# Kernel tuning notes

Measured on AMD Instinct MI355X. Metric: run time of the kernel, lower is better.

The kernel has to match this reference:

```python
import jax, jax.numpy as jnp
import numpy as np

SYM_LIST = np.array([12, 15, 18, 19, 20], dtype=np.int32)   # symmetric class ids (dataset.get_sym_list())
SELECT_ID = np.arange(1, 31, dtype=np.int32)                 # self.select_id = [1..30]
STEP = 20                                                     # pixel subsampling stride
SCORING_WEIGHT = 0.01


def quat_to_mat(q):
    """Exact translation of get_loss.quaternion_matrix. q: [..., 4] -> [..., 3, 3]."""
    q0, q1, q2, q3 = q[..., 0], q[..., 1], q[..., 2], q[..., 3]
    R = jnp.stack([
        1.0 - 2.0 * (q2 ** 2 + q3 ** 2), 2.0 * q1 * q2 - 2.0 * q0 * q3, 2.0 * q0 * q2 + 2.0 * q1 * q3,
        2.0 * q1 * q2 + 2.0 * q3 * q0, 1.0 - 2.0 * (q1 ** 2 + q3 ** 2), -2.0 * q0 * q1 + 2.0 * q2 * q3,
        -2.0 * q0 * q2 + 2.0 * q1 * q3, 2.0 * q0 * q1 + 2.0 * q2 * q3, 1.0 - 2.0 * (q1 ** 2 + q2 ** 2),
    ], axis=-1)
    return R.reshape(q.shape[:-1] + (3, 3))


def setup_inputs() -> dict:
    key = jax.random.key(0)
    ks = jax.random.split(key, 7)
    bs, h, w, P = 8, 64, 64, 400
    pred_r = jax.random.normal(ks[0], (bs, 4, h, w), jnp.float32)
    pred_t = jax.random.normal(ks[1], (bs, 3, h, w), jnp.float32) * 0.1
    pred_score = jax.random.uniform(ks[2], (bs, h, w), jnp.float32, 1e-3, 1.0)
    gt_r = jax.random.normal(ks[3], (bs, 3, 3), jnp.float32)
    gt_t = jax.random.normal(ks[4], (bs, 3), jnp.float32) * 0.1
    cls_ids = jax.random.randint(ks[5], (bs,), 0, 30, jnp.int32)
    model_xyz = jax.random.normal(ks[6], (bs, 3, P), jnp.float32) * 0.05
    return {"pred_r": pred_r, "pred_t": pred_t, "pred_score": pred_score,
            "gt_r": gt_r, "gt_t": gt_t, "cls_ids": cls_ids, "model_xyz": model_xyz}


def reference(pred_r, pred_t, pred_score, gt_r, gt_t, cls_ids, model_xyz):
    bs, _, h, w = pred_r.shape
    hw = h * w
    # per-pixel quaternion normalization
    pred_r = pred_r / jnp.linalg.norm(pred_r, axis=1, keepdims=True)
    pr = pred_r.reshape(bs, 4, hw)
    pt = pred_t.reshape(bs, 3, hw)
    ps = pred_score.reshape(bs, hw)
    # static strided subsampling of valid pixels (full mask -> every STEP-th pixel)
    V = hw // STEP
    idx = jnp.arange(V) * STEP
    pr = pr[:, :, idx]                 # [bs,4,V]
    pt = pt[:, :, idx]                 # [bs,3,V]
    ps = ps[:, idx]                    # [bs,V]
    R_pre = quat_to_mat(jnp.moveaxis(pr, 1, 2))                       # [bs,V,3,3]
    # transformed model points per valid pixel
    pred = jnp.einsum('bvij,bjp->bvip', R_pre, model_xyz) \
        + jnp.moveaxis(pt, 1, 2)[..., None]                           # [bs,V,3,P]
    gt = jnp.einsum('bij,bjp->bip', gt_r, model_xyz) + gt_t[..., None]  # [bs,3,P]
    # ADD: same-index point distances
    add = jnp.mean(jnp.linalg.norm(pred - gt[:, None], axis=2), axis=2)  # [bs,V]
    # ADD-S: nearest-neighbor (knn_one_point + gather == min over gt points)
    pn = jnp.sum(pred ** 2, axis=2)                                    # [bs,V,P]
    gn = jnp.sum(gt ** 2, axis=1)                                      # [bs,P]
    cross = jnp.einsum('bvip,biq->bvpq', pred, gt)                     # [bs,V,P,P]
    d2 = pn[..., None] + gn[:, None, None, :] - 2.0 * cross
    adds = jnp.mean(jnp.sqrt(jnp.maximum(jnp.min(d2, axis=-1), 0.0)), axis=2)  # [bs,V]
    is_sym = jnp.isin(cls_ids, jnp.asarray(SYM_LIST))                  # [bs]
    add_ij = jnp.where(is_sym[:, None], adds, add)                     # [bs,V]
    valid = jnp.isin(cls_ids + 1, jnp.asarray(SELECT_ID))              # cls+1 in select_id
    sub_value = jnp.where(valid, jnp.mean(add_ij, axis=1), 0.0)
    sub_loss = jnp.where(valid,
                         jnp.mean(add_ij * ps - SCORING_WEIGHT * jnp.log(ps), axis=1), 0.0)
    gadd_loss = jnp.mean(sub_loss)
    gadd = jnp.mean(sub_value)
    bad = jnp.isinf(gadd_loss) | jnp.isnan(gadd_loss)
    gadd_loss = jnp.where(bad, 0.0, gadd_loss)
    return gadd_loss + 0.0 * gadd
```

## Files before the change

### kernel.cpp

```cpp
#include <hip/hip_runtime.h>
#include <math.h>

#define NP 400
#define NV 204
#define STEP 20
#define HW 4096
#define BS 8
#define NBLK (NV * BS)

__global__ __launch_bounds__(256) void partial_kernel(
    const float* __restrict__ pred_r,
    const float* __restrict__ pred_t,
    const float* __restrict__ pred_score,
    const float* __restrict__ gt_r,
    const float* __restrict__ gt_t,
    const int*   __restrict__ cls_ids,
    const float* __restrict__ model_xyz,
    float* __restrict__ partials)
{
    const int v   = blockIdx.x;
    const int b   = blockIdx.y;
    const int tid = threadIdx.x;
    const int pix = v * STEP;

    __shared__ float4 s_g[NP];
    __shared__ float  s_part[4];

    const int   cls = cls_ids[b];
    const bool  sym = (cls==12)||(cls==15)||(cls==18)||(cls==19)||(cls==20);
    const bool  valid = (cls+1 >= 1) && (cls+1 <= 30);
    const bool  has2 = (tid < NP - 256);

    const float* mb = model_xyz + (size_t)b * 3 * NP;

    {
        const float g00 = gt_r[b*9+0], g01 = gt_r[b*9+1], g02 = gt_r[b*9+2];
        const float g10 = gt_r[b*9+3], g11 = gt_r[b*9+4], g12 = gt_r[b*9+5];
        const float g20 = gt_r[b*9+6], g21 = gt_r[b*9+7], g22 = gt_r[b*9+8];
        const float gtx = gt_t[b*3+0], gty = gt_t[b*3+1], gtz = gt_t[b*3+2];
        for (int q = tid; q < NP; q += 256) {
            float mx = mb[q], my = mb[NP+q], mz = mb[2*NP+q];
            float gx = g00*mx + g01*my + g02*mz + gtx;
            float gy = g10*mx + g11*my + g12*mz + gty;
            float gz = g20*mx + g21*my + g22*mz + gtz;
            s_g[q] = make_float4(gx, gy, gz, gx*gx + gy*gy + gz*gz);
        }
    }

    float q0 = pred_r[((size_t)b*4+0)*HW + pix];
    float q1 = pred_r[((size_t)b*4+1)*HW + pix];
    float q2 = pred_r[((size_t)b*4+2)*HW + pix];
    float q3 = pred_r[((size_t)b*4+3)*HW + pix];
    {
        float inv = 1.0f / sqrtf(q0*q0 + q1*q1 + q2*q2 + q3*q3);
        q0 *= inv; q1 *= inv; q2 *= inv; q3 *= inv;
    }
    const float R00 = 1.0f - 2.0f*(q2*q2 + q3*q3);
    const float R01 = 2.0f*q1*q2 - 2.0f*q0*q3;
    const float R02 = 2.0f*q0*q2 + 2.0f*q1*q3;
    const float R10 = 2.0f*q1*q2 + 2.0f*q3*q0;
    const float R11 = 1.0f - 2.0f*(q1*q1 + q3*q3);
    const float R12 = -2.0f*q0*q1 + 2.0f*q2*q3;
    const float R20 = -2.0f*q0*q2 + 2.0f*q1*q3;
    const float R21 = 2.0f*q0*q1 + 2.0f*q2*q3;
    const float R22 = 1.0f - 2.0f*(q1*q1 + q2*q2);

    const float ptx = pred_t[((size_t)b*3+0)*HW + pix];
    const float pty = pred_t[((size_t)b*3+1)*HW + pix];
    const float ptz = pred_t[((size_t)b*3+2)*HW + pix];

    __syncthreads();

    const int p0 = tid;
    const int p1 = has2 ? tid + 256 : tid;
    float mx0 = mb[p0], my0 = mb[NP+p0], mz0 = mb[2*NP+p0];
    float mx1 = mb[p1], my1 = mb[NP+p1], mz1 = mb[2*NP+p1];
    const float px0 = R00*mx0 + R01*my0 + R02*mz0 + ptx;
    const float py0 = R10*mx0 + R11*my0 + R12*mz0 + pty;
    const float pz0 = R20*mx0 + R21*my0 + R22*mz0 + ptz;
    const float px1 = R00*mx1 + R01*my1 + R02*mz1 + ptx;
    const float py1 = R10*mx1 + R11*my1 + R12*mz1 + pty;
    const float pz1 = R20*mx1 + R21*my1 + R22*mz1 + ptz;

    float d2_0 = 0.0f, d2_1 = 0.0f;
    if (sym) {
        const float nx0 = -2.0f*px0, ny0 = -2.0f*py0, nz0 = -2.0f*pz0;
        const float pn0 = px0*px0 + py0*py0 + pz0*pz0;
        if (tid < 192) {
            const float nx1 = -2.0f*px1, ny1 = -2.0f*py1, nz1 = -2.0f*pz1;
            const float pn1 = px1*px1 + py1*py1 + pz1*pz1;
            float a0 = 3.4e38f, a1 = 3.4e38f, a2 = 3.4e38f, a3 = 3.4e38f;
            float c0 = 3.4e38f, c1 = 3.4e38f, c2 = 3.4e38f, c3 = 3.4e38f;
            for (int q = 0; q < NP; q += 4) {
                const float4 g0 = s_g[q+0], g1 = s_g[q+1];
                const float4 g2 = s_g[q+2], g3 = s_g[q+3];
                a0 = fminf(a0, fmaf(nx0, g0.x, fmaf(ny0, g0.y, fmaf(nz0, g0.z, g0.w))));
                a1 = fminf(a1, fmaf(nx0, g1.x, fmaf(ny0, g1.y, fmaf(nz0, g1.z, g1.w))));
                a2 = fminf(a2, fmaf(nx0, g2.x, fmaf(ny0, g2.y, fmaf(nz0, g2.z, g2.w))));
                a3 = fminf(a3, fmaf(nx0, g3.x, fmaf(ny0, g3.y, fmaf(nz0, g3.z, g3.w))));
                c0 = fminf(c0, fmaf(nx1, g0.x, fmaf(ny1, g0.y, fmaf(nz1, g0.z, g0.w))));
                c1 = fminf(c1, fmaf(nx1, g1.x, fmaf(ny1, g1.y, fmaf(nz1, g1.z, g1.w))));
                c2 = fminf(c2, fmaf(nx1, g2.x, fmaf(ny1, g2.y, fmaf(nz1, g2.z, g2.w))));
                c3 = fminf(c3, fmaf(nx1, g3.x, fmaf(ny1, g3.y, fmaf(nz1, g3.z, g3.w))));
            }
            d2_0 = fmaxf(pn0 + fminf(fminf(a0, a1), fminf(a2, a3)), 0.0f);
            d2_1 = fmaxf(pn1 + fminf(fminf(c0, c1), fminf(c2, c3)), 0.0f);
        } else {
            float a0 = 3.4e38f, a1 = 3.4e38f, a2 = 3.4e38f, a3 = 3.4e38f;
            for (int q = 0; q < NP; q += 4) {
                const float4 g0 = s_g[q+0], g1 = s_g[q+1];
                const float4 g2 = s_g[q+2], g3 = s_g[q+3];
                a0 = fminf(a0, fmaf(nx0, g0.x, fmaf(ny0, g0.y, fmaf(nz0, g0.z, g0.w))));
                a1 = fminf(a1, fmaf(nx0, g1.x, fmaf(ny0, g1.y, fmaf(nz0, g1.z, g1.w))));
                a2 = fminf(a2, fmaf(nx0, g2.x, fmaf(ny0, g2.y, fmaf(nz0, g2.z, g2.w))));
                a3 = fminf(a3, fmaf(nx0, g3.x, fmaf(ny0, g3.y, fmaf(nz0, g3.z, g3.w))));
            }
            d2_0 = fmaxf(pn0 + fminf(fminf(a0, a1), fminf(a2, a3)), 0.0f);
            d2_1 = 0.0f;
        }
    } else {
        float4 g = s_g[p0];
        float dx = px0 - g.x, dy = py0 - g.y, dz = pz0 - g.z;
        d2_0 = dx*dx + dy*dy + dz*dz;
        g = s_g[p1];
        dx = px1 - g.x; dy = py1 - g.y; dz = pz1 - g.z;
        d2_1 = dx*dx + dy*dy + dz*dz;
    }
    float local = sqrtf(d2_0) + (has2 ? sqrtf(d2_1) : 0.0f);

    #pragma unroll
    for (int off = 32; off > 0; off >>= 1)
        local += __shfl_down(local, off, 64);
    const int wave = tid >> 6;
    if ((tid & 63) == 0) s_part[wave] = local;
    __syncthreads();
    if (tid == 0) {
        float tot  = s_part[0] + s_part[1] + s_part[2] + s_part[3];
        float mean = tot * (1.0f / NP);
        float ps   = pred_score[(size_t)b*HW + pix];
        float c = 0.0f;
        if (valid)
            c = (mean * ps - 0.01f * logf(ps)) * (1.0f / NBLK);
        partials[b * NV + v] = c;
    }
}

__global__ __launch_bounds__(256) void finalize_kernel(
    const float* __restrict__ partials, float* __restrict__ out)
{
    __shared__ float s_part[4];
    const int tid = threadIdx.x;
    const float4* p4 = reinterpret_cast<const float4*>(partials);
    float local = 0.0f;
    for (int i = tid; i < NBLK / 4; i += 256) {
        float4 vv = p4[i];
        local += vv.x + vv.y + vv.z + vv.w;
    }
    #pragma unroll
    for (int off = 32; off > 0; off >>= 1)
        local += __shfl_down(local, off, 64);
    if ((tid & 63) == 0) s_part[tid >> 6] = local;
    __syncthreads();
    if (tid == 0) {
        float vv = s_part[0] + s_part[1] + s_part[2] + s_part[3];
        if (isnan(vv) || isinf(vv)) vv = 0.0f;
        out[0] = vv;
    }
}

extern "C" void kernel_launch(void* const* d_in, const int* in_sizes, int n_in,
                              void* d_out, int out_size, void* d_ws, size_t ws_size,
                              hipStream_t stream) {
    const float* pred_r     = (const float*)d_in[0];
    const float* pred_t     = (const float*)d_in[1];
    const float* pred_score = (const float*)d_in[2];
    const float* gt_r       = (const float*)d_in[3];
    const float* gt_t       = (const float*)d_in[4];
    const int*   cls_ids    = (const int*)d_in[5];
    const float* model_xyz  = (const float*)d_in[6];
    float* out      = (float*)d_out;
    float* partials = (float*)d_ws;

    dim3 grid(NV, BS);
    partial_kernel<<<grid, 256, 0, stream>>>(pred_r, pred_t, pred_score,
                                             gt_r, gt_t, cls_ids, model_xyz, partials);
    finalize_kernel<<<1, 256, 0, stream>>>(partials, out);
}
```

Before: 70.80 us.

## Precompute transformed GT points once per batch and fuse finalize via last-block counter

Moves the per-batch ground-truth point transform into a small pre-kernel that writes to workspace, so the main kernel no longer rebuilds them in LDS per block and needs no barrier before the distance loop. The nearest-neighbour loop now reads the points from global memory (L1/L2-cached) instead of LDS. The separate finalize kernel is replaced by an atomic counter, and the last block to finish does the final reduction. This trades per-block LDS setup plus one kernel launch for an extra small launch, cached global reads in the inner loop, and atomics.

After: 116.3 us. 64.3% more time.

```diff
diff --git a/kernel.cpp b/kernel.cpp
--- a/kernel.cpp
+++ b/kernel.cpp
@@ -8,44 +8,59 @@
 #define BS 8
 #define NBLK (NV * BS)
 
-__global__ __launch_bounds__(256) void partial_kernel(
+
+__global__ __launch_bounds__(256) void pre_kernel(
+    const float* __restrict__ gt_r,
+    const float* __restrict__ gt_t,
+    const float* __restrict__ model_xyz,
+    float4* __restrict__ gw,
+    unsigned* __restrict__ counter)
+{
+    const int b   = blockIdx.x;
+    const int tid = threadIdx.x;
+    if (b == 0 && tid == 0) *counter = 0u;
+
+    const float g00 = gt_r[b*9+0], g01 = gt_r[b*9+1], g02 = gt_r[b*9+2];
+    const float g10 = gt_r[b*9+3], g11 = gt_r[b*9+4], g12 = gt_r[b*9+5];
+    const float g20 = gt_r[b*9+6], g21 = gt_r[b*9+7], g22 = gt_r[b*9+8];
+    const float gtx = gt_t[b*3+0], gty = gt_t[b*3+1], gtz = gt_t[b*3+2];
+    const float* mb = model_xyz + (size_t)b * 3 * NP;
+
+    for (int q = tid; q < NP; q += 256) {
+        float mx = mb[q], my = mb[NP+q], mz = mb[2*NP+q];
+        float gx = g00*mx + g01*my + g02*mz + gtx;
+        float gy = g10*mx + g11*my + g12*mz + gty;
+        float gz = g20*mx + g21*my + g22*mz + gtz;
+        gw[b*NP + q] = make_float4(gx, gy, gz, gx*gx + gy*gy + gz*gz);
+    }
+}
+
+__global__ __launch_bounds__(256) void main_kernel(
     const float* __restrict__ pred_r,
     const float* __restrict__ pred_t,
     const float* __restrict__ pred_score,
-    const float* __restrict__ gt_r,
-    const float* __restrict__ gt_t,
     const int*   __restrict__ cls_ids,
     const float* __restrict__ model_xyz,
-    float* __restrict__ partials)
+    const float4* __restrict__ gw,
+    float* __restrict__ partials,
+    unsigned* __restrict__ counter,
+    float* __restrict__ out)
 {
     const int v   = blockIdx.x;
     const int b   = blockIdx.y;
     const int tid = threadIdx.x;
     const int pix = v * STEP;
 
-    __shared__ float4 s_g[NP];
-    __shared__ float  s_part[4];
+    __shared__ float s_part[4];
+    __shared__ int   s_last;
 
-    const int   cls = cls_ids[b];
-    const bool  sym = (cls==12)||(cls==15)||(cls==18)||(cls==19)||(cls==20);
-    const bool  valid = (cls+1 >= 1) && (cls+1 <= 30);
-    const bool  has2 = (tid < NP - 256);
+    const int  cls   = cls_ids[b];
+    const bool sym   = (cls==12)||(cls==15)||(cls==18)||(cls==19)||(cls==20);
+    const bool valid = (cls+1 >= 1) && (cls+1 <= 30);
+    const bool has2  = (tid < NP - 256);
 
-    const float* mb = model_xyz + (size_t)b * 3 * NP;
-
-    {
-        const float g00 = gt_r[b*9+0], g01 = gt_r[b*9+1], g02 = gt_r[b*9+2];
-        const float g10 = gt_r[b*9+3], g11 = gt_r[b*9+4], g12 = gt_r[b*9+5];
-        const float g20 = gt_r[b*9+6], g21 = gt_r[b*9+7], g22 = gt_r[b*9+8];
-        const float gtx = gt_t[b*3+0], gty = gt_t[b*3+1], gtz = gt_t[b*3+2];
-        for (int q = tid; q < NP; q += 256) {
-            float mx = mb[q], my = mb[NP+q], mz = mb[2*NP+q];
-            float gx = g00*mx + g01*my + g02*mz + gtx;
-            float gy = g10*mx + g11*my + g12*mz + gty;
-            float gz = g20*mx + g21*my + g22*mz + gtz;
-            s_g[q] = make_float4(gx, gy, gz, gx*gx + gy*gy + gz*gz);
-        }
-    }
+    const float*  mb  = model_xyz + (size_t)b * 3 * NP;
+    const float4* gwb = gw + b * NP;
 
     float q0 = pred_r[((size_t)b*4+0)*HW + pix];
     float q1 = pred_r[((size_t)b*4+1)*HW + pix];
@@ -69,8 +84,6 @@
     const float pty = pred_t[((size_t)b*3+1)*HW + pix];
     const float ptz = pred_t[((size_t)b*3+2)*HW + pix];
 
-    __syncthreads();
-
     const int p0 = tid;
     const int p1 = has2 ? tid + 256 : tid;
     float mx0 = mb[p0], my0 = mb[NP+p0], mz0 = mb[2*NP+p0];
@@ -82,47 +95,33 @@
     const float py1 = R10*mx1 + R11*my1 + R12*mz1 + pty;
     const float pz1 = R20*mx1 + R21*my1 + R22*mz1 + ptz;
 
-    float d2_0 = 0.0f, d2_1 = 0.0f;
+    float d2_0, d2_1;
     if (sym) {
         const float nx0 = -2.0f*px0, ny0 = -2.0f*py0, nz0 = -2.0f*pz0;
         const float pn0 = px0*px0 + py0*py0 + pz0*pz0;
-        if (tid < 192) {
-            const float nx1 = -2.0f*px1, ny1 = -2.0f*py1, nz1 = -2.0f*pz1;
-            const float pn1 = px1*px1 + py1*py1 + pz1*pz1;
-            float a0 = 3.4e38f, a1 = 3.4e38f, a2 = 3.4e38f, a3 = 3.4e38f;
-            float c0 = 3.4e38f, c1 = 3.4e38f, c2 = 3.4e38f, c3 = 3.4e38f;
-            for (int q = 0; q < NP; q += 4) {
-                const float4 g0 = s_g[q+0], g1 = s_g[q+1];
-                const float4 g2 = s_g[q+2], g3 = s_g[q+3];
-                a0 = fminf(a0, fmaf(nx0, g0.x, fmaf(ny0, g0.y, fmaf(nz0, g0.z, g0.w))));
-                a1 = fminf(a1, fmaf(nx0, g1.x, fmaf(ny0, g1.y, fmaf(nz0, g1.z, g1.w))));
-                a2 = fminf(a2, fmaf(nx0, g2.x, fmaf(ny0, g2.y, fmaf(nz0, g2.z, g2.w))));
-                a3 = fminf(a3, fmaf(nx0, g3.x, fmaf(ny0, g3.y, fmaf(nz0, g3.z, g3.w))));
-                c0 = fminf(c0, fmaf(nx1, g0.x, fmaf(ny1, g0.y, fmaf(nz1, g0.z, g0.w))));
-                c1 = fminf(c1, fmaf(nx1, g1.x, fmaf(ny1, g1.y, fmaf(nz1, g1.z, g1.w))));
-                c2 = fminf(c2, fmaf(nx1, g2.x, fmaf(ny1, g2.y, fmaf(nz1, g2.z, g2.w))));
-                c3 = fminf(c3, fmaf(nx1, g3.x, fmaf(ny1, g3.y, fmaf(nz1, g3.z, g3.w))));
-            }
-            d2_0 = fmaxf(pn0 + fminf(fminf(a0, a1), fminf(a2, a3)), 0.0f);
-            d2_1 = fmaxf(pn1 + fminf(fminf(c0, c1), fminf(c2, c3)), 0.0f);
-        } else {
-            float a0 = 3.4e38f, a1 = 3.4e38f, a2 = 3.4e38f, a3 = 3.4e38f;
-            for (int q = 0; q < NP; q += 4) {
-                const float4 g0 = s_g[q+0], g1 = s_g[q+1];
-                const float4 g2 = s_g[q+2], g3 = s_g[q+3];
-                a0 = fminf(a0, fmaf(nx0, g0.x, fmaf(ny0, g0.y, fmaf(nz0, g0.z, g0.w))));
-                a1 = fminf(a1, fmaf(nx0, g1.x, fmaf(ny0, g1.y, fmaf(nz0, g1.z, g1.w))));
-                a2 = fminf(a2, fmaf(nx0, g2.x, fmaf(ny0, g2.y, fmaf(nz0, g2.z, g2.w))));
-                a3 = fminf(a3, fmaf(nx0, g3.x, fmaf(ny0, g3.y, fmaf(nz0, g3.z, g3.w))));
-            }
-            d2_0 = fmaxf(pn0 + fminf(fminf(a0, a1), fminf(a2, a3)), 0.0f);
-            d2_1 = 0.0f;
+        const float nx1 = -2.0f*px1, ny1 = -2.0f*py1, nz1 = -2.0f*pz1;
+        const float pn1 = px1*px1 + py1*py1 + pz1*pz1;
+        float a0 = 3.4e38f, a1 = 3.4e38f, a2 = 3.4e38f, a3 = 3.4e38f;
+        float c0 = 3.4e38f, c1 = 3.4e38f, c2 = 3.4e38f, c3 = 3.4e38f;
+        for (int q = 0; q < NP; q += 4) {
+            const float4 g0 = gwb[q+0], g1 = gwb[q+1];
+            const float4 g2 = gwb[q+2], g3 = gwb[q+3];
+            a0 = fminf(a0, fmaf(nx0, g0.x, fmaf(ny0, g0.y, fmaf(nz0, g0.z, g0.w))));
+            a1 = fminf(a1, fmaf(nx0, g1.x, fmaf(ny0, g1.y, fmaf(nz0, g1.z, g1.w))));
+            a2 = fminf(a2, fmaf(nx0, g2.x, fmaf(ny0, g2.y, fmaf(nz0, g2.z, g2.w))));
+            a3 = fminf(a3, fmaf(nx0, g3.x, fmaf(ny0, g3.y, fmaf(nz0, g3.z, g3.w))));
+            c0 = fminf(c0, fmaf(nx1, g0.x, fmaf(ny1, g0.y, fmaf(nz1, g0.z, g0.w))));
+            c1 = fminf(c1, fmaf(nx1, g1.x, fmaf(ny1, g1.y, fmaf(nz1, g1.z, g1.w))));
+            c2 = fminf(c2, fmaf(nx1, g2.x, fmaf(ny1, g2.y, fmaf(nz1, g2.z, g2.w))));
+            c3 = fminf(c3, fmaf(nx1, g3.x, fmaf(ny1, g3.y, fmaf(nz1, g3.z, g3.w))));
         }
+        d2_0 = fmaxf(pn0 + fminf(fminf(a0, a1), fminf(a2, a3)), 0.0f);
+        d2_1 = fmaxf(pn1 + fminf(fminf(c0, c1), fminf(c2, c3)), 0.0f);
     } else {
-        float4 g = s_g[p0];
+        float4 g = gwb[p0];
         float dx = px0 - g.x, dy = py0 - g.y, dz = pz0 - g.z;
         d2_0 = dx*dx + dy*dy + dz*dz;
-        g = s_g[p1];
+        g = gwb[p1];
         dx = px1 - g.x; dy = py1 - g.y; dz = pz1 - g.z;
         d2_1 = dx*dx + dy*dy + dz*dz;
     }
@@ -134,6 +133,7 @@
     const int wave = tid >> 6;
     if ((tid & 63) == 0) s_part[wave] = local;
     __syncthreads();
+
     if (tid == 0) {
         float tot  = s_part[0] + s_part[1] + s_part[2] + s_part[3];
         float mean = tot * (1.0f / NP);
@@ -141,30 +141,29 @@
         float c = 0.0f;
         if (valid)
             c = (mean * ps - 0.01f * logf(ps)) * (1.0f / NBLK);
-        partials[b * NV + v] = c;
+        __hip_atomic_store(&partials[b * NV + v], c,
+                           __ATOMIC_RELEASE, __HIP_MEMORY_SCOPE_AGENT);
+        unsigned prev = __hip_atomic_fetch_add(counter, 1u,
+                           __ATOMIC_ACQ_REL, __HIP_MEMORY_SCOPE_AGENT);
+        s_last = (prev == NBLK - 1) ? 1 : 0;
     }
-}
+    __syncthreads();
 
-__global__ __launch_bounds__(256) void finalize_kernel(
-    const float* __restrict__ partials, float* __restrict__ out)
-{
-    __shared__ float s_part[4];
-    const int tid = threadIdx.x;
-    const float4* p4 = reinterpret_cast<const float4*>(partials);
-    float local = 0.0f;
-    for (int i = tid; i < NBLK / 4; i += 256) {
-        float4 vv = p4[i];
-        local += vv.x + vv.y + vv.z + vv.w;
-    }
-    #pragma unroll
-    for (int off = 32; off > 0; off >>= 1)
-        local += __shfl_down(local, off, 64);
-    if ((tid & 63) == 0) s_part[tid >> 6] = local;
-    __syncthreads();
-    if (tid == 0) {
-        float vv = s_part[0] + s_part[1] + s_part[2] + s_part[3];
-        if (isnan(vv) || isinf(vv)) vv = 0.0f;
-        out[0] = vv;
+    if (s_last) {
+        float acc = 0.0f;
+        for (int i = tid; i < NBLK; i += 256)
+            acc += __hip_atomic_load(&partials[i],
+                       __ATOMIC_RELAXED, __HIP_MEMORY_SCOPE_AGENT);
+        #pragma unroll
+        for (int off = 32; off > 0; off >>= 1)
+            acc += __shfl_down(acc, off, 64);
+        if ((tid & 63) == 0) s_part[tid >> 6] = acc;
+        __syncthreads();
+        if (tid == 0) {
+            float vv = s_part[0] + s_part[1] + s_part[2] + s_part[3];
+            if (isnan(vv) || isinf(vv)) vv = 0.0f;
+            out[0] = vv;
+        }
     }
 }
 
@@ -178,11 +177,15 @@
     const float* gt_t       = (const float*)d_in[4];
     const int*   cls_ids    = (const int*)d_in[5];
     const float* model_xyz  = (const float*)d_in[6];
-    float* out      = (float*)d_out;
-    float* partials = (float*)d_ws;
+    float* out = (float*)d_out;
+
+    unsigned* counter  = (unsigned*)d_ws;
+    float4*   gw       = (float4*)((char*)d_ws + 64);
+    float*    partials = (float*)((char*)d_ws + 64 + (size_t)BS * NP * sizeof(float4));
+
+    pre_kernel<<<dim3(BS), 256, 0, stream>>>(gt_r, gt_t, model_xyz, gw, counter);
 
     dim3 grid(NV, BS);
-    partial_kernel<<<grid, 256, 0, stream>>>(pred_r, pred_t, pred_score,
-                                             gt_r, gt_t, cls_ids, model_xyz, partials);
-    finalize_kernel<<<1, 256, 0, stream>>>(partials, out);
+    main_kernel<<<grid, 256, 0, stream>>>(pred_r, pred_t, pred_score, cls_ids,
+                                          model_xyz, gw, partials, counter, out);
 }
```

## Register-tile symmetric NN search and skip shared staging for non-symmetric classes

Applied to the files above, without the earlier changes.

For symmetric classes, the nearest-neighbour search is restructured. Each group of 4 threads now owns about 6-7 predicted points held in registers, and each thread in the group scans an interleaved quarter of the 400 ground-truth points, with a shuffle-min across the group at the end. This raises the number of points reused per shared-memory load and balances work across threads, replacing the old uneven one-or-two-points-per-thread split. For non-symmetric classes, the transformed ground-truth points are computed in registers directly, so the shared-memory write and barrier are skipped. The cost is more registers and an extra shared array for the predicted points.

Result: no change. 69.52 us (-1.8%).

```diff
diff --git a/kernel.cpp b/kernel.cpp
--- a/kernel.cpp
+++ b/kernel.cpp
@@ -7,6 +7,7 @@
 #define HW 4096
 #define BS 8
 #define NBLK (NV * BS)
+
 
 __global__ __launch_bounds__(256) void partial_kernel(
     const float* __restrict__ pred_r,
@@ -24,6 +25,7 @@
     const int pix = v * STEP;
 
     __shared__ float4 s_g[NP];
+    __shared__ float4 s_p[NP];
     __shared__ float  s_part[4];
 
     const int   cls = cls_ids[b];
@@ -33,19 +35,22 @@
 
     const float* mb = model_xyz + (size_t)b * 3 * NP;
 
-    {
-        const float g00 = gt_r[b*9+0], g01 = gt_r[b*9+1], g02 = gt_r[b*9+2];
-        const float g10 = gt_r[b*9+3], g11 = gt_r[b*9+4], g12 = gt_r[b*9+5];
-        const float g20 = gt_r[b*9+6], g21 = gt_r[b*9+7], g22 = gt_r[b*9+8];
-        const float gtx = gt_t[b*3+0], gty = gt_t[b*3+1], gtz = gt_t[b*3+2];
-        for (int q = tid; q < NP; q += 256) {
-            float mx = mb[q], my = mb[NP+q], mz = mb[2*NP+q];
-            float gx = g00*mx + g01*my + g02*mz + gtx;
-            float gy = g10*mx + g11*my + g12*mz + gty;
-            float gz = g20*mx + g21*my + g22*mz + gtz;
-            s_g[q] = make_float4(gx, gy, gz, gx*gx + gy*gy + gz*gz);
-        }
-    }
+    const int p0 = tid;
+    const int p1 = has2 ? tid + 256 : tid;
+    const float mx0 = mb[p0], my0 = mb[NP+p0], mz0 = mb[2*NP+p0];
+    const float mx1 = mb[p1], my1 = mb[NP+p1], mz1 = mb[2*NP+p1];
+
+    const float g00 = gt_r[b*9+0], g01 = gt_r[b*9+1], g02 = gt_r[b*9+2];
+    const float g10 = gt_r[b*9+3], g11 = gt_r[b*9+4], g12 = gt_r[b*9+5];
+    const float g20 = gt_r[b*9+6], g21 = gt_r[b*9+7], g22 = gt_r[b*9+8];
+    const float gtx = gt_t[b*3+0], gty = gt_t[b*3+1], gtz = gt_t[b*3+2];
+
+    const float gx0 = g00*mx0 + g01*my0 + g02*mz0 + gtx;
+    const float gy0 = g10*mx0 + g11*my0 + g12*mz0 + gty;
+    const float gz0 = g20*mx0 + g21*my0 + g22*mz0 + gtz;
+    const float gx1 = g00*mx1 + g01*my1 + g02*mz1 + gtx;
+    const float gy1 = g10*mx1 + g11*my1 + g12*mz1 + gty;
+    const float gz1 = g20*mx1 + g21*my1 + g22*mz1 + gtz;
 
     float q0 = pred_r[((size_t)b*4+0)*HW + pix];
     float q1 = pred_r[((size_t)b*4+1)*HW + pix];
@@ -69,12 +74,6 @@
     const float pty = pred_t[((size_t)b*3+1)*HW + pix];
     const float ptz = pred_t[((size_t)b*3+2)*HW + pix];
 
-    __syncthreads();
-
-    const int p0 = tid;
-    const int p1 = has2 ? tid + 256 : tid;
-    float mx0 = mb[p0], my0 = mb[NP+p0], mz0 = mb[2*NP+p0];
-    float mx1 = mb[p1], my1 = mb[NP+p1], mz1 = mb[2*NP+p1];
     const float px0 = R00*mx0 + R01*my0 + R02*mz0 + ptx;
     const float py0 = R10*mx0 + R11*my0 + R12*mz0 + pty;
     const float pz0 = R20*mx0 + R21*my0 + R22*mz0 + ptz;
@@ -82,51 +81,59 @@
     const float py1 = R10*mx1 + R11*my1 + R12*mz1 + pty;
     const float pz1 = R20*mx1 + R21*my1 + R22*mz1 + ptz;
 
-    float d2_0 = 0.0f, d2_1 = 0.0f;
+    float local = 0.0f;
     if (sym) {
-        const float nx0 = -2.0f*px0, ny0 = -2.0f*py0, nz0 = -2.0f*pz0;
-        const float pn0 = px0*px0 + py0*py0 + pz0*pz0;
-        if (tid < 192) {
-            const float nx1 = -2.0f*px1, ny1 = -2.0f*py1, nz1 = -2.0f*pz1;
-            const float pn1 = px1*px1 + py1*py1 + pz1*pz1;
-            float a0 = 3.4e38f, a1 = 3.4e38f, a2 = 3.4e38f, a3 = 3.4e38f;
-            float c0 = 3.4e38f, c1 = 3.4e38f, c2 = 3.4e38f, c3 = 3.4e38f;
-            for (int q = 0; q < NP; q += 4) {
-                const float4 g0 = s_g[q+0], g1 = s_g[q+1];
-                const float4 g2 = s_g[q+2], g3 = s_g[q+3];
-                a0 = fminf(a0, fmaf(nx0, g0.x, fmaf(ny0, g0.y, fmaf(nz0, g0.z, g0.w))));
-                a1 = fminf(a1, fmaf(nx0, g1.x, fmaf(ny0, g1.y, fmaf(nz0, g1.z, g1.w))));
-                a2 = fminf(a2, fmaf(nx0, g2.x, fmaf(ny0, g2.y, fmaf(nz0, g2.z, g2.w))));
-                a3 = fminf(a3, fmaf(nx0, g3.x, fmaf(ny0, g3.y, fmaf(nz0, g3.z, g3.w))));
-                c0 = fminf(c0, fmaf(nx1, g0.x, fmaf(ny1, g0.y, fmaf(nz1, g0.z, g0.w))));
-                c1 = fminf(c1, fmaf(nx1, g1.x, fmaf(ny1, g1.y, fmaf(nz1, g1.z, g1.w))));
-                c2 = fminf(c2, fmaf(nx1, g2.x, fmaf(ny1, g2.y, fmaf(nz1, g2.z, g2.w))));
-                c3 = fminf(c3, fmaf(nx1, g3.x, fmaf(ny1, g3.y, fmaf(nz1, g3.z, g3.w))));
+        s_g[p0] = make_float4(gx0, gy0, gz0, gx0*gx0 + gy0*gy0 + gz0*gz0);
+        s_p[p0] = make_float4(px0, py0, pz0, px0*px0 + py0*py0 + pz0*pz0);
+        if (has2) {
+            s_g[p1] = make_float4(gx1, gy1, gz1, gx1*gx1 + gy1*gy1 + gz1*gz1);
+            s_p[p1] = make_float4(px1, py1, pz1, px1*px1 + py1*py1 + pz1*pz1);
+        }
+        __syncthreads();
+
+        const int sub    = tid & 3;
+        const int grp    = tid >> 2;
+        const int pstart = (25 * grp) >> 2;
+        const int pcount = ((25 * (grp + 1)) >> 2) - pstart;
+
+        float nx[7], ny[7], nz[7], pn[7], acc[7];
+        #pragma unroll
+        for (int j = 0; j < 7; ++j) {
+            const int pp = pstart + (j < pcount ? j : 0);
+            const float4 P = s_p[pp];
+            nx[j] = -2.0f * P.x;
+            ny[j] = -2.0f * P.y;
+            nz[j] = -2.0f * P.z;
+            pn[j] = P.w;
+            acc[j] = 3.4e38f;
+        }
+
+        for (int qb = 0; qb < NP; qb += 8) {
+            const float4 ga = s_g[qb + sub];
+            const float4 gb = s_g[qb + 4 + sub];
+            #pragma unroll
+            for (int j = 0; j < 7; ++j) {
+                const float da = fmaf(nx[j], ga.x, fmaf(ny[j], ga.y, fmaf(nz[j], ga.z, ga.w)));
+                const float db = fmaf(nx[j], gb.x, fmaf(ny[j], gb.y, fmaf(nz[j], gb.z, gb.w)));
+                acc[j] = fminf(acc[j], fminf(da, db));
             }
-            d2_0 = fmaxf(pn0 + fminf(fminf(a0, a1), fminf(a2, a3)), 0.0f);
-            d2_1 = fmaxf(pn1 + fminf(fminf(c0, c1), fminf(c2, c3)), 0.0f);
-        } else {
-            float a0 = 3.4e38f, a1 = 3.4e38f, a2 = 3.4e38f, a3 = 3.4e38f;
-            for (int q = 0; q < NP; q += 4) {
-                const float4 g0 = s_g[q+0], g1 = s_g[q+1];
-                const float4 g2 = s_g[q+2], g3 = s_g[q+3];
-                a0 = fminf(a0, fmaf(nx0, g0.x, fmaf(ny0, g0.y, fmaf(nz0, g0.z, g0.w))));
-                a1 = fminf(a1, fmaf(nx0, g1.x, fmaf(ny0, g1.y, fmaf(nz0, g1.z, g1.w))));
-                a2 = fminf(a2, fmaf(nx0, g2.x, fmaf(ny0, g2.y, fmaf(nz0, g2.z, g2.w))));
-                a3 = fminf(a3, fmaf(nx0, g3.x, fmaf(ny0, g3.y, fmaf(nz0, g3.z, g3.w))));
-            }
-            d2_0 = fmaxf(pn0 + fminf(fminf(a0, a1), fminf(a2, a3)), 0.0f);
-            d2_1 = 0.0f;
+        }
+
+        #pragma unroll
+        for (int j = 0; j < 7; ++j) {
+            float m = acc[j];
+            m = fminf(m, __shfl_xor(m, 1, 64));
+            m = fminf(m, __shfl_xor(m, 2, 64));
+            if (sub == 0 && j < pcount)
+                local += sqrtf(fmaxf(pn[j] + m, 0.0f));
         }
     } else {
-        float4 g = s_g[p0];
-        float dx = px0 - g.x, dy = py0 - g.y, dz = pz0 - g.z;
-        d2_0 = dx*dx + dy*dy + dz*dz;
-        g = s_g[p1];
-        dx = px1 - g.x; dy = py1 - g.y; dz = pz1 - g.z;
-        d2_1 = dx*dx + dy*dy + dz*dz;
+        float dx = px0 - gx0, dy = py0 - gy0, dz = pz0 - gz0;
+        const float d2_0 = dx*dx + dy*dy + dz*dz;
+        dx = px1 - gx1; dy = py1 - gy1; dz = pz1 - gz1;
+        const float d2_1 = dx*dx + dy*dy + dz*dz;
+        local = sqrtf(d2_0) + (has2 ? sqrtf(d2_1) : 0.0f);
     }
-    float local = sqrtf(d2_0) + (has2 ? sqrtf(d2_1) : 0.0f);
 
     #pragma unroll
     for (int off = 32; off > 0; off >>= 1)
```
